# Optimization experiments

Hardware: AMD Instinct MI355X
Metric: run time of the kernel (lower is better)

The kernel has to match this reference:

```python
import jax, jax.numpy as jnp
import numpy as np

# Dims: M=batch, T=time frames, B=bottleneck channels, H=intermediate channels, KK=kernel size
M, T, B, H, KK = 8, 4000, 128, 512, 3
DILATION = 2
EPS = 1e-8  # gLN eps (ConvTasNet convention)


def prelu(x, a):
    return jnp.where(x >= 0, x, a * x)


def gln(x, gamma, beta):
    # global layer norm over (time, channel) per sample; x: [M, T, C]
    m = jnp.mean(x, axis=(1, 2), keepdims=True)
    v = jnp.mean((x - m) ** 2, axis=(1, 2), keepdims=True)
    return gamma * (x - m) / jnp.sqrt(v + EPS) + beta


def depthwise_conv_same_reflect(x, w):
    # x: [M, C, L], w: [C, K]; dilation 1, 'same' padding with reflect mode
    K = w.shape[1]
    pl = (K - 1) // 2
    xp = jnp.pad(x, ((0, 0), (0, 0), (pl, K - 1 - pl)), mode='reflect')
    return jax.lax.conv_general_dilated(
        xp, w[:, None, :], (1,), 'VALID',
        feature_group_count=x.shape[1], dimension_numbers=('NCH', 'OIH', 'NCH'))


def setup_inputs() -> dict:
    key = jax.random.key(0)
    ks = jax.random.split(key, 12)
    f32 = jnp.float32
    return {
        'x': jax.random.normal(ks[0], (M, T, B), f32),
        'conv1_w': jax.random.normal(ks[1], (H, B), f32) * 0.05,
        'prelu1_a': jnp.asarray(0.25, f32),
        'norm1_g': jnp.ones((H,), f32),
        'norm1_b': jnp.zeros((H,), f32),
        'off_dw_w': jax.random.normal(ks[2], (H, KK), f32) * 0.02,
        'odc_prelu_a': jnp.asarray(0.25, f32),
        'off_pw_w': jax.random.normal(ks[3], (KK, H), f32) * 0.02,
        'opc_prelu_a': jnp.asarray(0.25, f32),
        'dw_w': jax.random.normal(ks[4], (H, KK), f32) * 0.05,
        'dw_b': jax.random.normal(ks[5], (H,), f32) * 0.01,
        'prelu2_a': jnp.asarray(0.25, f32),
        'norm2_g': jnp.ones((H,), f32),
        'norm2_b': jnp.zeros((H,), f32),
        'pw_w': jax.random.normal(ks[6], (B, H), f32) * 0.05,
    }


def reference(x, conv1_w, prelu1_a, norm1_g, norm1_b,
              off_dw_w, odc_prelu_a, off_pw_w, opc_prelu_a,
              dw_w, dw_b, prelu2_a, norm2_g, norm2_b, pw_w):
    dtype = x.dtype
    residual = x
    # 1x1 bottleneck conv -> PReLU -> gLN
    h = jnp.einsum('mtb,hb->mth', x, conv1_w)
    h = gln(prelu(h, prelu1_a), norm1_g, norm1_b)
    hc = jnp.moveaxis(h, 1, 2)  # [M, H, T]

    # --- offset prediction branch (PackedDeformConv1d) ---
    off = depthwise_conv_same_reflect(hc, off_dw_w)          # [M, H, T]
    off = prelu(off, odc_prelu_a)
    off = jnp.einsum('mct,kc->mkt', off, off_pw_w)           # [M, KK, T]
    off = prelu(off, opc_prelu_a)
    offsets = jnp.moveaxis(off, 1, 2)                        # [M, T, KK]

    # --- deformable depthwise conv (same padding, reflect) ---
    pad_tot = DILATION * (KK - 1)
    pl = pad_tot // 2
    xp = jnp.pad(hc, ((0, 0), (0, 0), (pl, pad_tot - pl)), mode='reflect')  # [M,H,Lp]
    Lp = T + pad_tot
    dil_pos = (jnp.arange(KK) * DILATION).astype(dtype)      # [KK]: 0, d, 2d
    t0 = jnp.arange(T, dtype=dtype)[:, None]                 # [T,1]
    Tpos = t0 + dil_pos[None, :] + offsets                   # [M,T,KK]
    Tpos = jnp.clip(Tpos, t0, t0 + dil_pos[-1])              # constrain to receptive field
    U = jnp.clip(jnp.floor(Tpos).astype(jnp.int32), 0, Lp - 2)
    Uf = U.astype(dtype)
    g0 = jax.nn.relu(1.0 - jnp.abs(Uf - Tpos))               # [M,T,KK]
    g1 = jax.nn.relu(1.0 - jnp.abs(Uf + 1.0 - Tpos))
    idx = jnp.broadcast_to(U.reshape(M, 1, T * KK), (M, H, T * KK))
    s0 = jnp.take_along_axis(xp, idx, axis=2).reshape(M, H, T, KK)
    s1 = jnp.take_along_axis(xp, idx + 1, axis=2).reshape(M, H, T, KK)
    sampled = g0[:, None] * s0 + g1[:, None] * s1            # [M,H,T,KK]
    y = jnp.einsum('mhtk,hk->mht', sampled, dw_w) + dw_b[None, :, None]

    # PReLU -> gLN -> 1x1 conv back to B channels, residual add
    y = jnp.moveaxis(y, 1, 2)                                # [M,T,H]
    y = gln(prelu(y, prelu2_a), norm2_g, norm2_b)
    out = jnp.einsum('mth,bh->mtb', y, pw_w)
    return out + residual
```

## Files before the change

kernel.cpp:

```cpp
#include <hip/hip_runtime.h>

#define Mdim 8
#define Tdim 4000
#define Bdim 128
#define Hdim 512
#define NPER (Tdim*Hdim)
#define EPSG 1e-8f

typedef __attribute__((ext_vector_type(8))) short short8;
typedef __attribute__((ext_vector_type(4))) float floatx4;

static __device__ __forceinline__ float bits2f(unsigned short s) {
  union { unsigned int u; float f; } v; v.u = ((unsigned int)s) << 16; return v.f;
}
static __device__ __forceinline__ unsigned short f2bits(float f) {
  union { float f; unsigned int u; } v; v.f = f;
  unsigned int u = v.u;
  u += 0x7fffu + ((u >> 16) & 1u);
  return (unsigned short)(u >> 16);
}
static __device__ __forceinline__ short8 pack8(const float4& a, const float4& b) {
  short8 v;
  v[0]=(short)f2bits(a.x); v[1]=(short)f2bits(a.y); v[2]=(short)f2bits(a.z); v[3]=(short)f2bits(a.w);
  v[4]=(short)f2bits(b.x); v[5]=(short)f2bits(b.y); v[6]=(short)f2bits(b.z); v[7]=(short)f2bits(b.w);
  return v;
}

__global__ __launch_bounds__(256) void k_reduce(
    const float2* __restrict__ part, int count, float* __restrict__ stats)
{
  __shared__ float rs[256], rq[256];
  const int m = blockIdx.x, tid = threadIdx.x;
  float s = 0.f, q = 0.f;
  for (int i = tid; i < count; i += 256) {
    float2 p = part[(size_t)m*count + i];
    s += p.x; q += p.y;
  }
  rs[tid] = s; rq[tid] = q;
  __syncthreads();
  for (int st = 128; st > 0; st >>= 1) {
    if (tid < st) { rs[tid] += rs[tid+st]; rq[tid] += rq[tid+st]; }
    __syncthreads();
  }
  if (tid == 0) { stats[m*2] = rs[0]; stats[m*2+1] = rq[0]; }
}

__global__ __launch_bounds__(256) void k_conv1(
    const float* __restrict__ x,
    const float* __restrict__ w1,
    const float* __restrict__ a1p,
    unsigned short* __restrict__ Hbuf,
    float2* __restrict__ part1)
{
  __shared__ __align__(16) unsigned short ldsW[64*136];
  __shared__ __align__(16) unsigned short ltile[64*72];
  __shared__ float red[512];

  const int tid = threadIdx.x;
  const int t0 = blockIdx.x * 64;
  const int h0 = blockIdx.y * 64;
  const int m  = blockIdx.z;

  #pragma unroll
  for (int it = 0; it < 4; ++it) {
    int idx = (it*256 + tid) * 8;
    int r = idx >> 7, c = idx & 127;
    float4 fa = *(const float4*)&w1[(size_t)(h0 + r)*Bdim + c];
    float4 fb = *(const float4*)&w1[(size_t)(h0 + r)*Bdim + c + 4];
    *(short8*)&ldsW[r*136 + c] = pack8(fa, fb);
  }

  const int lane = tid & 63, wv = tid >> 6, quad = lane >> 4, l16 = lane & 15;
  int tr = t0 + wv*16 + l16;
  int trc = tr < Tdim ? tr : Tdim-1;
  const float* xrow = x + ((size_t)m*Tdim + trc)*Bdim;
  short8 afr[4];
  #pragma unroll
  for (int ks = 0; ks < 4; ++ks) {
    float4 fa = *(const float4*)&xrow[ks*32 + quad*8];
    float4 fb = *(const float4*)&xrow[ks*32 + quad*8 + 4];
    afr[ks] = pack8(fa, fb);
  }

  floatx4 acc[4] = {};
  __syncthreads();
  #pragma unroll
  for (int ks = 0; ks < 4; ++ks) {
    #pragma unroll
    for (int nt = 0; nt < 4; ++nt) {
      short8 bfr = *(const short8*)&ldsW[(nt*16 + l16)*136 + ks*32 + quad*8];
      acc[nt] = __builtin_amdgcn_mfma_f32_16x16x32_bf16(afr[ks], bfr, acc[nt], 0, 0, 0);
    }
  }

  const float a1 = a1p[0];
  float lsum = 0.f, lss = 0.f;
  #pragma unroll
  for (int nt = 0; nt < 4; ++nt) {
    int hl = nt*16 + l16;
    #pragma unroll
    for (int r = 0; r < 4; ++r) {
      int tl = wv*16 + quad*4 + r;
      float v = acc[nt][r];
      v = v >= 0.f ? v : a1 * v;
      if (t0 + tl < Tdim) { lsum += v; lss += v*v; }
      ltile[tl*72 + hl] = f2bits(v);
    }
  }
  red[tid] = lsum; red[256 + tid] = lss;
  __syncthreads();
  {
    int tr2 = tid >> 2, ck = (tid & 3) * 16;
    int tg = t0 + tr2;
    if (tg < Tdim) {
      unsigned short* dst = &Hbuf[((size_t)m*Tdim + tg)*Hdim + h0 + ck];
      *(short8*)&dst[0] = *(const short8*)&ltile[tr2*72 + ck];
      *(short8*)&dst[8] = *(const short8*)&ltile[tr2*72 + ck + 8];
    }
  }
  for (int s = 128; s > 0; s >>= 1) {
    if (tid < s) { red[tid] += red[tid + s]; red[256+tid] += red[256+tid+s]; }
    __syncthreads();
  }
  if (tid == 0)
    part1[(size_t)m*504 + blockIdx.y*63 + blockIdx.x] = make_float2(red[0], red[256]);
}

__global__ __launch_bounds__(256) void k_offsets(
    const unsigned short* __restrict__ Hbuf,
    const float* __restrict__ stats1,
    const float* __restrict__ g1w,
    const float* __restrict__ b1w,
    const float* __restrict__ odw,
    const float* __restrict__ aodcp,
    const float* __restrict__ opw,
    float* __restrict__ OffAcc)
{
  const int tid = threadIdx.x, lane = tid & 63, w = tid >> 6;
  const int t = blockIdx.x*4 + w;
  const int m = blockIdx.y;
  const float invn = 1.0f/(float)NPER;
  const float mean1 = stats1[m*2]*invn;
  const float var1  = fmaxf(stats1[m*2+1]*invn - mean1*mean1, 0.f);
  const float inv1  = 1.0f/sqrtf(var1 + EPSG);
  const float aodc  = aodcp[0];

  const int c8 = lane*8;
  float g1v[8], b1v[8], wod[24], q0v[8], q1v[8], q2v[8];
  #pragma unroll
  for (int j = 0; j < 8; j += 4) {
    *(float4*)&g1v[j] = *(const float4*)&g1w[c8 + j];
    *(float4*)&b1v[j] = *(const float4*)&b1w[c8 + j];
    *(float4*)&q0v[j] = *(const float4*)&opw[c8 + j];
    *(float4*)&q1v[j] = *(const float4*)&opw[Hdim + c8 + j];
    *(float4*)&q2v[j] = *(const float4*)&opw[2*Hdim + c8 + j];
  }
  #pragma unroll
  for (int j = 0; j < 24; j += 4)
    *(float4*)&wod[j] = *(const float4*)&odw[c8*3 + j];

  const int tm1 = (t == 0) ? 1 : t-1;
  const int tp1 = (t == Tdim-1) ? Tdim-2 : t+1;
  const unsigned short* base = Hbuf + (size_t)m*Tdim*Hdim;
  short8 hm = *(const short8*)&base[(size_t)tm1*Hdim + c8];
  short8 hz = *(const short8*)&base[(size_t)t  *Hdim + c8];
  short8 hp = *(const short8*)&base[(size_t)tp1*Hdim + c8];

  float o0 = 0.f, o1 = 0.f, o2 = 0.f;
  #pragma unroll
  for (int j = 0; j < 8; ++j) {
    float A = g1v[j] * inv1;
    float C = b1v[j] - mean1*A;
    float fm = fmaf(A, bits2f((unsigned short)hm[j]), C);
    float fz = fmaf(A, bits2f((unsigned short)hz[j]), C);
    float fp = fmaf(A, bits2f((unsigned short)hp[j]), C);
    float d = fm*wod[j*3+0] + fz*wod[j*3+1] + fp*wod[j*3+2];
    d = d >= 0.f ? d : aodc*d;
    o0 = fmaf(d, q0v[j], o0);
    o1 = fmaf(d, q1v[j], o1);
    o2 = fmaf(d, q2v[j], o2);
  }
  #pragma unroll
  for (int s = 32; s > 0; s >>= 1) {
    o0 += __shfl_xor(o0, s);
    o1 += __shfl_xor(o1, s);
    o2 += __shfl_xor(o2, s);
  }
  if (lane == 0) {
    float* oa = OffAcc + ((size_t)m*Tdim + t)*3;
    oa[0] = o0; oa[1] = o1; oa[2] = o2;
  }
}

__global__ __launch_bounds__(256) void k_deform(
    const unsigned short* __restrict__ Hbuf,
    const float* __restrict__ stats1,
    const float* __restrict__ OffAcc,
    const float* __restrict__ g1w,
    const float* __restrict__ b1w,
    const float* __restrict__ aopcp,
    const float* __restrict__ dww,
    const float* __restrict__ dwb,
    const float* __restrict__ a2p,
    unsigned short* __restrict__ Ybuf,
    float2* __restrict__ part2)
{
  __shared__ float rsum[4], rss[4];
  const int tid = threadIdx.x, lane = tid & 63, w = tid >> 6;
  const int t = blockIdx.x*4 + w;
  const int m = blockIdx.y;

  const float invn = 1.0f/(float)NPER;
  const float mean1 = stats1[m*2]*invn;
  const float var1  = fmaxf(stats1[m*2+1]*invn - mean1*mean1, 0.f);
  const float inv1  = 1.0f/sqrtf(var1 + EPSG);
  const float aopc  = aopcp[0];
  const float a2    = a2p[0];

  int I0[3], I1[3]; float G0[3], G1[3], GS[3];
  const float tf = (float)t;
  #pragma unroll
  for (int k = 0; k < 3; ++k) {
    float off = OffAcc[((size_t)m*Tdim + t)*3 + k];
    off = off >= 0.f ? off : aopc*off;
    float pos = tf + (float)(2*k) + off;
    pos = fminf(fmaxf(pos, tf), tf + 4.0f);
    int U = (int)floorf(pos);
    if (U > Tdim + 2) U = Tdim + 2;
    float Uf = (float)U;
    G0[k] = fmaxf(0.f, 1.f - fabsf(Uf - pos));
    G1[k] = fmaxf(0.f, 1.f - fabsf(Uf + 1.f - pos));
    GS[k] = G0[k] + G1[k];
    int ia = U - 2; ia = ia < 0 ? -ia : ia; if (ia > Tdim-1) ia = 2*(Tdim-1) - ia;
    int ib = U - 1; ib = ib < 0 ? -ib : ib; if (ib > Tdim-1) ib = 2*(Tdim-1) - ib;
    I0[k] = ia; I1[k] = ib;
  }

  const int c8 = lane*8;
  const unsigned short* base = Hbuf + (size_t)m*Tdim*Hdim;
  short8 s0v[3], s1v[3];
  #pragma unroll
  for (int k = 0; k < 3; ++k) {
    s0v[k] = *(const short8*)&base[(size_t)I0[k]*Hdim + c8];
    s1v[k] = *(const short8*)&base[(size_t)I1[k]*Hdim + c8];
  }

  float g1v[8], b1v[8], bv[8], wd[24];
  #pragma unroll
  for (int j = 0; j < 8; j += 4) {
    *(float4*)&g1v[j] = *(const float4*)&g1w[c8 + j];
    *(float4*)&b1v[j] = *(const float4*)&b1w[c8 + j];
    *(float4*)&bv[j]  = *(const float4*)&dwb[c8 + j];
  }
  #pragma unroll
  for (int j = 0; j < 24; j += 4)
    *(float4*)&wd[j] = *(const float4*)&dww[c8*3 + j];

  float lsum = 0.f, lss = 0.f;
  short8 yv;
  #pragma unroll
  for (int j = 0; j < 8; ++j) {
    float A = g1v[j] * inv1;
    float C = b1v[j] - mean1*A;
    float w0 = wd[j*3+0], w1 = wd[j*3+1], w2 = wd[j*3+2];
    float ybase = fmaf(C, w0*GS[0] + w1*GS[1] + w2*GS[2], bv[j]);
    float t0s = fmaf(G1[0], bits2f((unsigned short)s1v[0][j]), G0[0]*bits2f((unsigned short)s0v[0][j]));
    float t1s = fmaf(G1[1], bits2f((unsigned short)s1v[1][j]), G0[1]*bits2f((unsigned short)s0v[1][j]));
    float t2s = fmaf(G1[2], bits2f((unsigned short)s1v[2][j]), G0[2]*bits2f((unsigned short)s0v[2][j]));
    float acc = w0*t0s + w1*t1s + w2*t2s;
    float y = fmaf(A, acc, ybase);
    float p = y >= 0.f ? y : a2*y;
    lsum += p; lss += p*p;
    yv[j] = (short)f2bits(p);
  }
  *(short8*)&Ybuf[((size_t)m*Tdim + t)*Hdim + c8] = yv;

  #pragma unroll
  for (int s = 32; s > 0; s >>= 1) {
    lsum += __shfl_xor(lsum, s);
    lss  += __shfl_xor(lss, s);
  }
  if (lane == 0) { rsum[w] = lsum; rss[w] = lss; }
  __syncthreads();
  if (tid == 0)
    part2[(size_t)m*1000 + blockIdx.x] =
      make_float2(rsum[0]+rsum[1]+rsum[2]+rsum[3], rss[0]+rss[1]+rss[2]+rss[3]);
}

__global__ __launch_bounds__(64) void k_w2(
    const float* __restrict__ stats2,
    const float* __restrict__ g2w,
    const float* __restrict__ b2w,
    const float* __restrict__ pww,
    unsigned short* __restrict__ W2,
    float* __restrict__ const2)
{
  const int bid = blockIdx.x;
  const int m = bid >> 7, b = bid & 127;
  const int tid = threadIdx.x;
  const float invn = 1.0f/(float)NPER;
  const float mean2 = stats2[m*2]*invn;
  const float var2  = fmaxf(stats2[m*2+1]*invn - mean2*mean2, 0.f);
  const float inv2  = 1.0f/sqrtf(var2 + EPSG);
  float csum = 0.f;
  for (int j = tid; j < Hdim; j += 64) {
    float A = g2w[j] * inv2;
    float C = b2w[j] - mean2*A;
    float wv = pww[(size_t)b*Hdim + j];
    W2[((size_t)m*Bdim + b)*Hdim + j] = f2bits(A*wv);
    csum = fmaf(C, wv, csum);
  }
  #pragma unroll
  for (int s = 32; s > 0; s >>= 1) csum += __shfl_down(csum, s);
  if (tid == 0) const2[m*Bdim + b] = csum;
}

__global__ __launch_bounds__(256) void k_out(
    const unsigned short* __restrict__ Ybuf,
    const unsigned short* __restrict__ W2,
    const float* __restrict__ const2,
    const float* __restrict__ x,
    float* __restrict__ out)
{
  __shared__ __align__(16) unsigned short ldsW[64*136];
  __shared__ __align__(16) float ltf[64*68];
  const int tid = threadIdx.x;
  const int t0 = blockIdx.x*64;
  const int n0 = blockIdx.y*64;
  const int m  = blockIdx.z;
  const int lane = tid & 63, wv = tid >> 6, quad = lane >> 4, l16 = lane & 15;
  int tr = t0 + wv*16 + l16;
  int trc = tr < Tdim ? tr : Tdim-1;
  const unsigned short* arow = Ybuf + ((size_t)m*Tdim + trc)*Hdim;
  floatx4 acc[4] = {};
  for (int kc = 0; kc < 4; ++kc) {
    __syncthreads();
    #pragma unroll
    for (int it = 0; it < 4; ++it) {
      int idx = (it*256 + tid)*8;
      int r = idx >> 7, c = idx & 127;
      *(short8*)&ldsW[r*136 + c] =
        *(const short8*)&W2[((size_t)m*Bdim + n0 + r)*Hdim + kc*128 + c];
    }
    __syncthreads();
    #pragma unroll
    for (int ks = 0; ks < 4; ++ks) {
      short8 afr = *(const short8*)&arow[kc*128 + ks*32 + quad*8];
      #pragma unroll
      for (int nt = 0; nt < 4; ++nt) {
        short8 bfr = *(const short8*)&ldsW[(nt*16 + l16)*136 + ks*32 + quad*8];
        acc[nt] = __builtin_amdgcn_mfma_f32_16x16x32_bf16(afr, bfr, acc[nt], 0, 0, 0);
      }
    }
  }
  __syncthreads();
  #pragma unroll
  for (int nt = 0; nt < 4; ++nt) {
    int bl = nt*16 + l16;
    float cb = const2[m*Bdim + n0 + bl];
    #pragma unroll
    for (int r = 0; r < 4; ++r) {
      int tl = wv*16 + quad*4 + r;
      ltf[tl*68 + bl] = acc[nt][r] + cb;
    }
  }
  __syncthreads();
  {
    int tr2 = tid >> 2, ck = (tid & 3) * 16;
    int tg = t0 + tr2;
    if (tg < Tdim) {
      const float* xr = &x[((size_t)m*Tdim + tg)*Bdim + n0 + ck];
      float* orow = &out[((size_t)m*Tdim + tg)*Bdim + n0 + ck];
      #pragma unroll
      for (int j = 0; j < 4; ++j) {
        float4 v = *(const float4*)&ltf[tr2*68 + ck + j*4];
        float4 rx = *(const float4*)&xr[j*4];
        v.x += rx.x; v.y += rx.y; v.z += rx.z; v.w += rx.w;
        *(float4*)&orow[j*4] = v;
      }
    }
  }
}

extern "C" void kernel_launch(void* const* d_in, const int* in_sizes, int n_in,
                              void* d_out, int out_size, void* d_ws, size_t ws_size,
                              hipStream_t stream)
{
  (void)in_sizes; (void)n_in; (void)out_size; (void)ws_size;
  const float* x    = (const float*)d_in[0];
  const float* w1   = (const float*)d_in[1];
  const float* a1   = (const float*)d_in[2];
  const float* g1   = (const float*)d_in[3];
  const float* b1   = (const float*)d_in[4];
  const float* odw  = (const float*)d_in[5];
  const float* aodc = (const float*)d_in[6];
  const float* opw  = (const float*)d_in[7];
  const float* aopc = (const float*)d_in[8];
  const float* dww  = (const float*)d_in[9];
  const float* dwb  = (const float*)d_in[10];
  const float* a2   = (const float*)d_in[11];
  const float* g2   = (const float*)d_in[12];
  const float* b2   = (const float*)d_in[13];
  const float* pww  = (const float*)d_in[14];
  float* out = (float*)d_out;

  char* ws = (char*)d_ws;
  const size_t OFF_S1 = 0;
  const size_t OFF_S2 = 64;
  const size_t OFF_C2 = 128;
  const size_t OFF_OF = 4224;
  const size_t OFF_P1 = 388224;
  const size_t OFF_P2 = 420480;
  const size_t OFF_W2 = 484480;
  const size_t OFF_H  = 1533056;
  const size_t OFF_Y  = 34301056;
  float*  stats1 = (float*)(ws + OFF_S1);
  float*  stats2 = (float*)(ws + OFF_S2);
  float*  const2 = (float*)(ws + OFF_C2);
  float*  OffAcc = (float*)(ws + OFF_OF);
  float2* part1  = (float2*)(ws + OFF_P1);
  float2* part2  = (float2*)(ws + OFF_P2);
  unsigned short* W2   = (unsigned short*)(ws + OFF_W2);
  unsigned short* Hbuf = (unsigned short*)(ws + OFF_H);
  unsigned short* Ybuf = (unsigned short*)(ws + OFF_Y);

  k_conv1  <<<dim3(63, 8, 8), 256, 0, stream>>>(x, w1, a1, Hbuf, part1);
  k_reduce <<<dim3(8), 256, 0, stream>>>(part1, 504, stats1);
  k_offsets<<<dim3(1000, 8), 256, 0, stream>>>(Hbuf, stats1, g1, b1, odw, aodc, opw, OffAcc);
  k_deform <<<dim3(1000, 8), 256, 0, stream>>>(Hbuf, stats1, OffAcc, g1, b1, aopc, dww, dwb, a2, Ybuf, part2);
  k_reduce <<<dim3(8), 256, 0, stream>>>(part2, 1000, stats2);
  k_w2     <<<dim3(1024), 64, 0, stream>>>(stats2, g2, b2, pww, W2, const2);
  k_out    <<<dim3(63, 2, 8), 256, 0, stream>>>(Ybuf, W2, const2, x, out);
}
```

Baseline: 191.3 us.

## Fuse offset prediction into deform kernel and fold stat reductions into consumers

Offset prediction now runs inside the deform kernel, so the OffAcc round trip and one launch go away. Both k_reduce launches are gone: the deform kernel and k_w2 each reduce the partial sums themselves. conv1 now loops over all 8 H-chunks per block, with 504 blocks instead of 4032, so each x row is loaded once and only 63 partials per sample are made. k_w2 is vectorised. The cost is less parallelism in conv1 and repeated partial reductions across many blocks.

```diff
diff --git a/kernel.cpp b/kernel.cpp
--- a/kernel.cpp
+++ b/kernel.cpp
@@ -24,25 +24,6 @@
   v[0]=(short)f2bits(a.x); v[1]=(short)f2bits(a.y); v[2]=(short)f2bits(a.z); v[3]=(short)f2bits(a.w);
   v[4]=(short)f2bits(b.x); v[5]=(short)f2bits(b.y); v[6]=(short)f2bits(b.z); v[7]=(short)f2bits(b.w);
   return v;
-}
-
-__global__ __launch_bounds__(256) void k_reduce(
-    const float2* __restrict__ part, int count, float* __restrict__ stats)
-{
-  __shared__ float rs[256], rq[256];
-  const int m = blockIdx.x, tid = threadIdx.x;
-  float s = 0.f, q = 0.f;
-  for (int i = tid; i < count; i += 256) {
-    float2 p = part[(size_t)m*count + i];
-    s += p.x; q += p.y;
-  }
-  rs[tid] = s; rq[tid] = q;
-  __syncthreads();
-  for (int st = 128; st > 0; st >>= 1) {
-    if (tid < st) { rs[tid] += rs[tid+st]; rq[tid] += rq[tid+st]; }
-    __syncthreads();
-  }
-  if (tid == 0) { stats[m*2] = rs[0]; stats[m*2+1] = rq[0]; }
 }
 
 __global__ __launch_bounds__(256) void k_conv1(
@@ -58,17 +39,7 @@
 
   const int tid = threadIdx.x;
   const int t0 = blockIdx.x * 64;
-  const int h0 = blockIdx.y * 64;
-  const int m  = blockIdx.z;
-
-  #pragma unroll
-  for (int it = 0; it < 4; ++it) {
-    int idx = (it*256 + tid) * 8;
-    int r = idx >> 7, c = idx & 127;
-    float4 fa = *(const float4*)&w1[(size_t)(h0 + r)*Bdim + c];
-    float4 fb = *(const float4*)&w1[(size_t)(h0 + r)*Bdim + c + 4];
-    *(short8*)&ldsW[r*136 + c] = pack8(fa, fb);
-  }
+  const int m  = blockIdx.y;
 
   const int lane = tid & 63, wv = tid >> 6, quad = lane >> 4, l16 = lane & 15;
   int tr = t0 + wv*16 + l16;
@@ -82,122 +53,74 @@
     afr[ks] = pack8(fa, fb);
   }
 
-  floatx4 acc[4] = {};
-  __syncthreads();
-  #pragma unroll
-  for (int ks = 0; ks < 4; ++ks) {
-    #pragma unroll
-    for (int nt = 0; nt < 4; ++nt) {
-      short8 bfr = *(const short8*)&ldsW[(nt*16 + l16)*136 + ks*32 + quad*8];
-      acc[nt] = __builtin_amdgcn_mfma_f32_16x16x32_bf16(afr[ks], bfr, acc[nt], 0, 0, 0);
-    }
-  }
-
   const float a1 = a1p[0];
   float lsum = 0.f, lss = 0.f;
-  #pragma unroll
-  for (int nt = 0; nt < 4; ++nt) {
-    int hl = nt*16 + l16;
-    #pragma unroll
-    for (int r = 0; r < 4; ++r) {
-      int tl = wv*16 + quad*4 + r;
-      float v = acc[nt][r];
-      v = v >= 0.f ? v : a1 * v;
-      if (t0 + tl < Tdim) { lsum += v; lss += v*v; }
-      ltile[tl*72 + hl] = f2bits(v);
-    }
-  }
+
+  for (int hc = 0; hc < 8; ++hc) {
+    const int h0 = hc * 64;
+    __syncthreads();
+    #pragma unroll
+    for (int it = 0; it < 4; ++it) {
+      int idx = (it*256 + tid) * 8;
+      int r = idx >> 7, c = idx & 127;
+      float4 fa = *(const float4*)&w1[(size_t)(h0 + r)*Bdim + c];
+      float4 fb = *(const float4*)&w1[(size_t)(h0 + r)*Bdim + c + 4];
+      *(short8*)&ldsW[r*136 + c] = pack8(fa, fb);
+    }
+    __syncthreads();
+
+    floatx4 acc[4] = {};
+    #pragma unroll
+    for (int ks = 0; ks < 4; ++ks) {
+      #pragma unroll
+      for (int nt = 0; nt < 4; ++nt) {
+        short8 bfr = *(const short8*)&ldsW[(nt*16 + l16)*136 + ks*32 + quad*8];
+        acc[nt] = __builtin_amdgcn_mfma_f32_16x16x32_bf16(afr[ks], bfr, acc[nt], 0, 0, 0);
+      }
+    }
+
+    #pragma unroll
+    for (int nt = 0; nt < 4; ++nt) {
+      int hl = nt*16 + l16;
+      #pragma unroll
+      for (int r = 0; r < 4; ++r) {
+        int tl = wv*16 + quad*4 + r;
+        float v = acc[nt][r];
+        v = v >= 0.f ? v : a1 * v;
+        if (t0 + tl < Tdim) { lsum += v; lss += v*v; }
+        ltile[tl*72 + hl] = f2bits(v);
+      }
+    }
+    __syncthreads();
+    {
+      int tr2 = tid >> 2, ck = (tid & 3) * 16;
+      int tg = t0 + tr2;
+      if (tg < Tdim) {
+        unsigned short* dst = &Hbuf[((size_t)m*Tdim + tg)*Hdim + h0 + ck];
+        *(short8*)&dst[0] = *(const short8*)&ltile[tr2*72 + ck];
+        *(short8*)&dst[8] = *(const short8*)&ltile[tr2*72 + ck + 8];
+      }
+    }
+  }
+
   red[tid] = lsum; red[256 + tid] = lss;
   __syncthreads();
-  {
-    int tr2 = tid >> 2, ck = (tid & 3) * 16;
-    int tg = t0 + tr2;
-    if (tg < Tdim) {
-      unsigned short* dst = &Hbuf[((size_t)m*Tdim + tg)*Hdim + h0 + ck];
-      *(short8*)&dst[0] = *(const short8*)&ltile[tr2*72 + ck];
-      *(short8*)&dst[8] = *(const short8*)&ltile[tr2*72 + ck + 8];
-    }
-  }
   for (int s = 128; s > 0; s >>= 1) {
     if (tid < s) { red[tid] += red[tid + s]; red[256+tid] += red[256+tid+s]; }
     __syncthreads();
   }
   if (tid == 0)
-    part1[(size_t)m*504 + blockIdx.y*63 + blockIdx.x] = make_float2(red[0], red[256]);
-}
-
-__global__ __launch_bounds__(256) void k_offsets(
+    part1[(size_t)m*63 + blockIdx.x] = make_float2(red[0], red[256]);
+}
+
+__global__ __launch_bounds__(256) void k_deform(
     const unsigned short* __restrict__ Hbuf,
-    const float* __restrict__ stats1,
+    const float2* __restrict__ part1,
     const float* __restrict__ g1w,
     const float* __restrict__ b1w,
     const float* __restrict__ odw,
     const float* __restrict__ aodcp,
     const float* __restrict__ opw,
-    float* __restrict__ OffAcc)
-{
-  const int tid = threadIdx.x, lane = tid & 63, w = tid >> 6;
-  const int t = blockIdx.x*4 + w;
-  const int m = blockIdx.y;
-  const float invn = 1.0f/(float)NPER;
-  const float mean1 = stats1[m*2]*invn;
-  const float var1  = fmaxf(stats1[m*2+1]*invn - mean1*mean1, 0.f);
-  const float inv1  = 1.0f/sqrtf(var1 + EPSG);
-  const float aodc  = aodcp[0];
-
-  const int c8 = lane*8;
-  float g1v[8], b1v[8], wod[24], q0v[8], q1v[8], q2v[8];
-  #pragma unroll
-  for (int j = 0; j < 8; j += 4) {
-    *(float4*)&g1v[j] = *(const float4*)&g1w[c8 + j];
-    *(float4*)&b1v[j] = *(const float4*)&b1w[c8 + j];
-    *(float4*)&q0v[j] = *(const float4*)&opw[c8 + j];
-    *(float4*)&q1v[j] = *(const float4*)&opw[Hdim + c8 + j];
-    *(float4*)&q2v[j] = *(const float4*)&opw[2*Hdim + c8 + j];
-  }
-  #pragma unroll
-  for (int j = 0; j < 24; j += 4)
-    *(float4*)&wod[j] = *(const float4*)&odw[c8*3 + j];
-
-  const int tm1 = (t == 0) ? 1 : t-1;
-  const int tp1 = (t == Tdim-1) ? Tdim-2 : t+1;
-  const unsigned short* base = Hbuf + (size_t)m*Tdim*Hdim;
-  short8 hm = *(const short8*)&base[(size_t)tm1*Hdim + c8];
-  short8 hz = *(const short8*)&base[(size_t)t  *Hdim + c8];
-  short8 hp = *(const short8*)&base[(size_t)tp1*Hdim + c8];
-
-  float o0 = 0.f, o1 = 0.f, o2 = 0.f;
-  #pragma unroll
-  for (int j = 0; j < 8; ++j) {
-    float A = g1v[j] * inv1;
-    float C = b1v[j] - mean1*A;
-    float fm = fmaf(A, bits2f((unsigned short)hm[j]), C);
-    float fz = fmaf(A, bits2f((unsigned short)hz[j]), C);
-    float fp = fmaf(A, bits2f((unsigned short)hp[j]), C);
-    float d = fm*wod[j*3+0] + fz*wod[j*3+1] + fp*wod[j*3+2];
-    d = d >= 0.f ? d : aodc*d;
-    o0 = fmaf(d, q0v[j], o0);
-    o1 = fmaf(d, q1v[j], o1);
-    o2 = fmaf(d, q2v[j], o2);
-  }
-  #pragma unroll
-  for (int s = 32; s > 0; s >>= 1) {
-    o0 += __shfl_xor(o0, s);
-    o1 += __shfl_xor(o1, s);
-    o2 += __shfl_xor(o2, s);
-  }
-  if (lane == 0) {
-    float* oa = OffAcc + ((size_t)m*Tdim + t)*3;
-    oa[0] = o0; oa[1] = o1; oa[2] = o2;
-  }
-}
-
-__global__ __launch_bounds__(256) void k_deform(
-    const unsigned short* __restrict__ Hbuf,
-    const float* __restrict__ stats1,
-    const float* __restrict__ OffAcc,
-    const float* __restrict__ g1w,
-    const float* __restrict__ b1w,
     const float* __restrict__ aopcp,
     const float* __restrict__ dww,
     const float* __restrict__ dwb,
@@ -205,39 +128,100 @@
     unsigned short* __restrict__ Ybuf,
     float2* __restrict__ part2)
 {
+  __shared__ float s_stats[2];
   __shared__ float rsum[4], rss[4];
   const int tid = threadIdx.x, lane = tid & 63, w = tid >> 6;
   const int t = blockIdx.x*4 + w;
   const int m = blockIdx.y;
 
+  if (tid < 64) {
+    float2 p = (lane < 63) ? part1[(size_t)m*63 + lane] : make_float2(0.f, 0.f);
+    float s = p.x, q = p.y;
+    #pragma unroll
+    for (int st = 32; st > 0; st >>= 1) { s += __shfl_xor(s, st); q += __shfl_xor(q, st); }
+    if (lane == 0) { s_stats[0] = s; s_stats[1] = q; }
+  }
+  __syncthreads();
   const float invn = 1.0f/(float)NPER;
-  const float mean1 = stats1[m*2]*invn;
-  const float var1  = fmaxf(stats1[m*2+1]*invn - mean1*mean1, 0.f);
+  const float mean1 = s_stats[0]*invn;
+  const float var1  = fmaxf(s_stats[1]*invn - mean1*mean1, 0.f);
   const float inv1  = 1.0f/sqrtf(var1 + EPSG);
-  const float aopc  = aopcp[0];
-  const float a2    = a2p[0];
-
-  int I0[3], I1[3]; float G0[3], G1[3], GS[3];
-  const float tf = (float)t;
-  #pragma unroll
-  for (int k = 0; k < 3; ++k) {
-    float off = OffAcc[((size_t)m*Tdim + t)*3 + k];
-    off = off >= 0.f ? off : aopc*off;
-    float pos = tf + (float)(2*k) + off;
-    pos = fminf(fmaxf(pos, tf), tf + 4.0f);
-    int U = (int)floorf(pos);
-    if (U > Tdim + 2) U = Tdim + 2;
-    float Uf = (float)U;
-    G0[k] = fmaxf(0.f, 1.f - fabsf(Uf - pos));
-    G1[k] = fmaxf(0.f, 1.f - fabsf(Uf + 1.f - pos));
-    GS[k] = G0[k] + G1[k];
-    int ia = U - 2; ia = ia < 0 ? -ia : ia; if (ia > Tdim-1) ia = 2*(Tdim-1) - ia;
-    int ib = U - 1; ib = ib < 0 ? -ib : ib; if (ib > Tdim-1) ib = 2*(Tdim-1) - ib;
-    I0[k] = ia; I1[k] = ib;
-  }
 
   const int c8 = lane*8;
   const unsigned short* base = Hbuf + (size_t)m*Tdim*Hdim;
+
+  float g1v[8], b1v[8];
+  #pragma unroll
+  for (int j = 0; j < 8; j += 4) {
+    *(float4*)&g1v[j] = *(const float4*)&g1w[c8 + j];
+    *(float4*)&b1v[j] = *(const float4*)&b1w[c8 + j];
+  }
+
+  float o0 = 0.f, o1 = 0.f, o2 = 0.f;
+  {
+    const float aodc = aodcp[0];
+    float wod[24], q0v[8], q1v[8], q2v[8];
+    #pragma unroll
+    for (int j = 0; j < 8; j += 4) {
+      *(float4*)&q0v[j] = *(const float4*)&opw[c8 + j];
+      *(float4*)&q1v[j] = *(const float4*)&opw[Hdim + c8 + j];
+      *(float4*)&q2v[j] = *(const float4*)&opw[2*Hdim + c8 + j];
+    }
+    #pragma unroll
+    for (int j = 0; j < 24; j += 4)
+      *(float4*)&wod[j] = *(const float4*)&odw[c8*3 + j];
+
+    const int tm1 = (t == 0) ? 1 : t-1;
+    const int tp1 = (t == Tdim-1) ? Tdim-2 : t+1;
+    short8 hm = *(const short8*)&base[(size_t)tm1*Hdim + c8];
+    short8 hz = *(const short8*)&base[(size_t)t  *Hdim + c8];
+    short8 hp = *(const short8*)&base[(size_t)tp1*Hdim + c8];
+
+    #pragma unroll
+    for (int j = 0; j < 8; ++j) {
+      float A = g1v[j] * inv1;
+      float C = b1v[j] - mean1*A;
+      float fm = fmaf(A, bits2f((unsigned short)hm[j]), C);
+      float fz = fmaf(A, bits2f((unsigned short)hz[j]), C);
+      float fp = fmaf(A, bits2f((unsigned short)hp[j]), C);
+      float d = fm*wod[j*3+0] + fz*wod[j*3+1] + fp*wod[j*3+2];
+      d = d >= 0.f ? d : aodc*d;
+      o0 = fmaf(d, q0v[j], o0);
+      o1 = fmaf(d, q1v[j], o1);
+      o2 = fmaf(d, q2v[j], o2);
+    }
+    #pragma unroll
+    for (int s = 32; s > 0; s >>= 1) {
+      o0 += __shfl_xor(o0, s);
+      o1 += __shfl_xor(o1, s);
+      o2 += __shfl_xor(o2, s);
+    }
+  }
+
+  const float aopc = aopcp[0];
+  const float a2   = a2p[0];
+  int I0[3], I1[3]; float G0[3], G1[3], GS[3];
+  {
+    const float tf = (float)t;
+    float offs[3] = {o0, o1, o2};
+    #pragma unroll
+    for (int k = 0; k < 3; ++k) {
+      float off = offs[k];
+      off = off >= 0.f ? off : aopc*off;
+      float pos = tf + (float)(2*k) + off;
+      pos = fminf(fmaxf(pos, tf), tf + 4.0f);
+      int U = (int)floorf(pos);
+      if (U > Tdim + 2) U = Tdim + 2;
+      float Uf = (float)U;
+      G0[k] = fmaxf(0.f, 1.f - fabsf(Uf - pos));
+      G1[k] = fmaxf(0.f, 1.f - fabsf(Uf + 1.f - pos));
+      GS[k] = G0[k] + G1[k];
+      int ia = U - 2; ia = ia < 0 ? -ia : ia; if (ia > Tdim-1) ia = 2*(Tdim-1) - ia;
+      int ib = U - 1; ib = ib < 0 ? -ib : ib; if (ib > Tdim-1) ib = 2*(Tdim-1) - ib;
+      I0[k] = ia; I1[k] = ib;
+    }
+  }
+
   short8 s0v[3], s1v[3];
   #pragma unroll
   for (int k = 0; k < 3; ++k) {
@@ -245,13 +229,10 @@
     s1v[k] = *(const short8*)&base[(size_t)I1[k]*Hdim + c8];
   }
 
-  float g1v[8], b1v[8], bv[8], wd[24];
-  #pragma unroll
-  for (int j = 0; j < 8; j += 4) {
-    *(float4*)&g1v[j] = *(const float4*)&g1w[c8 + j];
-    *(float4*)&b1v[j] = *(const float4*)&b1w[c8 + j];
-    *(float4*)&bv[j]  = *(const float4*)&dwb[c8 + j];
-  }
+  float bv[8], wd[24];
+  #pragma unroll
+  for (int j = 0; j < 8; j += 4)
+    *(float4*)&bv[j] = *(const float4*)&dwb[c8 + j];
   #pragma unroll
   for (int j = 0; j < 24; j += 4)
     *(float4*)&wd[j] = *(const float4*)&dww[c8*3 + j];
@@ -288,7 +269,7 @@
 }
 
 __global__ __launch_bounds__(64) void k_w2(
-    const float* __restrict__ stats2,
+    const float2* __restrict__ part2,
     const float* __restrict__ g2w,
     const float* __restrict__ b2w,
     const float* __restrict__ pww,
@@ -298,20 +279,41 @@
   const int bid = blockIdx.x;
   const int m = bid >> 7, b = bid & 127;
   const int tid = threadIdx.x;
+
+  float s = 0.f, q = 0.f;
+  for (int i = tid; i < 1000; i += 64) {
+    float2 p = part2[(size_t)m*1000 + i];
+    s += p.x; q += p.y;
+  }
+  #pragma unroll
+  for (int st = 32; st > 0; st >>= 1) { s += __shfl_xor(s, st); q += __shfl_xor(q, st); }
+
   const float invn = 1.0f/(float)NPER;
-  const float mean2 = stats2[m*2]*invn;
-  const float var2  = fmaxf(stats2[m*2+1]*invn - mean2*mean2, 0.f);
+  const float mean2 = s*invn;
+  const float var2  = fmaxf(q*invn - mean2*mean2, 0.f);
   const float inv2  = 1.0f/sqrtf(var2 + EPSG);
+
+  const int j8 = tid*8;
+  float g2v[8], b2v[8], pv[8];
+  #pragma unroll
+  for (int j = 0; j < 8; j += 4) {
+    *(float4*)&g2v[j] = *(const float4*)&g2w[j8 + j];
+    *(float4*)&b2v[j] = *(const float4*)&b2w[j8 + j];
+    *(float4*)&pv[j]  = *(const float4*)&pww[(size_t)b*Hdim + j8 + j];
+  }
   float csum = 0.f;
-  for (int j = tid; j < Hdim; j += 64) {
-    float A = g2w[j] * inv2;
-    float C = b2w[j] - mean2*A;
-    float wv = pww[(size_t)b*Hdim + j];
-    W2[((size_t)m*Bdim + b)*Hdim + j] = f2bits(A*wv);
-    csum = fmaf(C, wv, csum);
-  }
-  #pragma unroll
-  for (int s = 32; s > 0; s >>= 1) csum += __shfl_down(csum, s);
+  short8 wv8;
+  #pragma unroll
+  for (int j = 0; j < 8; ++j) {
+    float A = g2v[j] * inv2;
+    float C = b2v[j] - mean2*A;
+    csum = fmaf(C, pv[j], csum);
+    wv8[j] = (short)f2bits(A*pv[j]);
+  }
+  *(short8*)&W2[((size_t)m*Bdim + b)*Hdim + j8] = wv8;
+
+  #pragma unroll
+  for (int st = 32; st > 0; st >>= 1) csum += __shfl_down(csum, st);
   if (tid == 0) const2[m*Bdim + b] = csum;
 }
 
@@ -405,30 +407,21 @@
   float* out = (float*)d_out;
 
   char* ws = (char*)d_ws;
-  const size_t OFF_S1 = 0;
-  const size_t OFF_S2 = 64;
-  const size_t OFF_C2 = 128;
-  const size_t OFF_OF = 4224;
-  const size_t OFF_P1 = 388224;
-  const size_t OFF_P2 = 420480;
-  const size_t OFF_W2 = 484480;
-  const size_t OFF_H  = 1533056;
-  const size_t OFF_Y  = 34301056;
-  float*  stats1 = (float*)(ws + OFF_S1);
-  float*  stats2 = (float*)(ws + OFF_S2);
+  const size_t OFF_P1 = 0;
+  const size_t OFF_C2 = 4096;
+  const size_t OFF_P2 = 8192;
+  const size_t OFF_W2 = 72192;
+  const size_t OFF_H  = 1120768;
+  const size_t OFF_Y  = 33888768;
+  float2* part1  = (float2*)(ws + OFF_P1);
   float*  const2 = (float*)(ws + OFF_C2);
-  float*  OffAcc = (float*)(ws + OFF_OF);
-  float2* part1  = (float2*)(ws + OFF_P1);
   float2* part2  = (float2*)(ws + OFF_P2);
   unsigned short* W2   = (unsigned short*)(ws + OFF_W2);
   unsigned short* Hbuf = (unsigned short*)(ws + OFF_H);
   unsigned short* Ybuf = (unsigned short*)(ws + OFF_Y);
 
-  k_conv1  <<<dim3(63, 8, 8), 256, 0, stream>>>(x, w1, a1, Hbuf, part1);
-  k_reduce <<<dim3(8), 256, 0, stream>>>(part1, 504, stats1);
-  k_offsets<<<dim3(1000, 8), 256, 0, stream>>>(Hbuf, stats1, g1, b1, odw, aodc, opw, OffAcc);
-  k_deform <<<dim3(1000, 8), 256, 0, stream>>>(Hbuf, stats1, OffAcc, g1, b1, aopc, dww, dwb, a2, Ybuf, part2);
-  k_reduce <<<dim3(8), 256, 0, stream>>>(part2, 1000, stats2);
-  k_w2     <<<dim3(1024), 64, 0, stream>>>(stats2, g2, b2, pww, W2, const2);
-  k_out    <<<dim3(63, 2, 8), 256, 0, stream>>>(Ybuf, W2, const2, x, out);
-}
+  k_conv1 <<<dim3(63, 8), 256, 0, stream>>>(x, w1, a1, Hbuf, part1);
+  k_deform<<<dim3(1000, 8), 256, 0, stream>>>(Hbuf, part1, g1, b1, odw, aodc, opw, aopc, dww, dwb, a2, Ybuf, part2);
+  k_w2    <<<dim3(1024), 64, 0, stream>>>(part2, g2, b2, pww, W2, const2);
+  k_out   <<<dim3(63, 2, 8), 256, 0, stream>>>(Ybuf, W2, const2, x, out);
+}
```

Result: faster. 178.5 us (-6.7%).
